# Optimization experiments

Measured on AMD Instinct MI355X. Metric: run time of the kernel, lower is better.

## Reference

```python
import jax, jax.numpy as jnp
import numpy as np

HEADS = 16
HEAD_DIM = 64
EMB = 1024
B, S = 4, 2048
SCALE = 1.0 / 8.0  # fixed constant in the original code
MASK_PENALTY = -50.0  # original adds -50 * upper_triangular, not -inf


def setup_inputs() -> dict:
    key = jax.random.key(0)
    ks = jax.random.split(key, 5)
    x = jax.random.normal(ks[0], (B, S, EMB), dtype=jnp.float32)
    Wq = jax.random.normal(ks[1], (EMB, HEADS * HEAD_DIM), dtype=jnp.float32) * 0.02
    Wk = jax.random.normal(ks[2], (EMB, HEADS * HEAD_DIM), dtype=jnp.float32) * 0.02
    Wv = jax.random.normal(ks[3], (EMB, HEADS * HEAD_DIM), dtype=jnp.float32) * 0.02
    Wr = jax.random.normal(ks[4], (HEADS * HEAD_DIM, EMB), dtype=jnp.float32) * 0.02
    return {"x": x, "Wq": Wq, "Wk": Wk, "Wv": Wv, "Wr": Wr}


def reference(x, Wq, Wk, Wv, Wr):
    b, s, _ = x.shape
    # project and split heads: [b, s, h, d]
    q = (x @ Wq).reshape(b, s, HEADS, HEAD_DIM)
    k = (x @ Wk).reshape(b, s, HEADS, HEAD_DIM)
    v = (x @ Wv).reshape(b, s, HEADS, HEAD_DIM)
    # scores: [b, h, s, s]
    scores = SCALE * jnp.einsum('bqhd,bkhd->bhqk', q, k)
    # causal additive mask: -50 on strictly-upper triangle (faithful to original)
    causal = jnp.triu(jnp.ones((s, s), dtype=x.dtype), k=1)
    scores = scores + MASK_PENALTY * causal
    attn = jax.nn.softmax(scores, axis=-1)
    out = jnp.einsum('bhqk,bkhd->bqhd', attn, v).reshape(b, s, HEADS * HEAD_DIM)
    return out @ Wr
```

## Files before the change

### kernel.cpp

```cpp
#include <hip/hip_runtime.h>

typedef _Float16 f16;
typedef _Float16 f16x8 __attribute__((ext_vector_type(8)));
typedef _Float16 f16x4 __attribute__((ext_vector_type(4)));
typedef float f32x4 __attribute__((ext_vector_type(4)));

#define MFMA16(A, B, C) __builtin_amdgcn_mfma_f32_16x16x32_f16((A), (B), (C), 0, 0, 0)

__device__ __forceinline__ void async16(void* lds, const void* gp) {
    __builtin_amdgcn_global_load_lds(
        (__attribute__((address_space(1))) void*)(gp),
        (__attribute__((address_space(3))) void*)(lds), 16, 0, 0);
}

__global__ __launch_bounds__(256) void k_convert(const float* __restrict__ in,
                                                 f16* __restrict__ out, int n) {
    int i = (blockIdx.x * 256 + threadIdx.x) * 4;
    if (i + 3 < n) {
        float4 v = *(const float4*)(in + i);
        f16x4 o = {(f16)v.x, (f16)v.y, (f16)v.z, (f16)v.w};
        *(f16x4*)(out + i) = o;
    }
}

__global__ __launch_bounds__(256) void k_transpose_w4(const float* __restrict__ Wq,
                                                      const float* __restrict__ Wk,
                                                      const float* __restrict__ Wv,
                                                      const float* __restrict__ Wr,
                                                      f16* __restrict__ Wqkvt,
                                                      f16* __restrict__ Wrt) {
    __shared__ float tile[32][33];
    int z = blockIdx.z;
    const float* W = (z == 0) ? Wq : (z == 1) ? Wk : (z == 2) ? Wv : Wr;
    f16* Wt = (z == 3) ? Wrt : Wqkvt + z * 1048576;
    int c0 = blockIdx.x * 32, r0 = blockIdx.y * 32;
    int tx = threadIdx.x, ty = threadIdx.y;
#pragma unroll
    for (int j = 0; j < 32; j += 8)
        tile[ty + j][tx] = W[(r0 + ty + j) * 1024 + c0 + tx];
    __syncthreads();
#pragma unroll
    for (int j = 0; j < 32; j += 8)
        Wt[(c0 + ty + j) * 1024 + r0 + tx] = (f16)tile[tx][ty + j];
}

__global__ __launch_bounds__(256) void k_transpose_v(const f16* __restrict__ QKV,
                                                     f16* __restrict__ Vt) {
    __shared__ f16 tile[32][33];
    int s0 = blockIdx.x * 32;
    int d0 = blockIdx.y * 32;
    int bh = blockIdx.z;
    int b = bh >> 4, h = bh & 15;
    int tx = threadIdx.x, ty = threadIdx.y;
#pragma unroll
    for (int j = 0; j < 32; j += 8)
        tile[ty + j][tx] = QKV[(b * 2048 + s0 + ty + j) * 3072 + 2048 + h * 64 + d0 + tx];
    __syncthreads();
#pragma unroll
    for (int j = 0; j < 32; j += 8)
        Vt[(bh * 64 + d0 + ty + j) * 2048 + s0 + tx] = tile[tx][ty + j];
}

template <bool OUT_F16>
__global__ __launch_bounds__(256) void k_gemm_bt(const f16* __restrict__ A,
                                                 const f16* __restrict__ Bt,
                                                 void* __restrict__ Cv,
                                                 int M, int N, int K) {
    __shared__ f16 As[128][32];
    __shared__ f16 Bs[128][32];
    int t = threadIdx.x;
    int lane = t & 63, w = t >> 6;
    int wm = (w >> 1) * 64, wn = (w & 1) * 64;
    int m0 = blockIdx.y * 128, n0 = blockIdx.x * 128;
    int ln = lane & 15, g = lane >> 4;

    int lin0 = w * 128 + lane, lin1 = lin0 + 64;
    int r0 = lin0 >> 2, c0 = (lin0 & 3) ^ ((r0 >> 1) & 3);
    int r1 = lin1 >> 2, c1 = (lin1 & 3) ^ ((r1 >> 1) & 3);
    const f16* gA0 = A + (size_t)(m0 + r0) * K + c0 * 8;
    const f16* gA1 = A + (size_t)(m0 + r1) * K + c1 * 8;
    const f16* gB0 = Bt + (size_t)(n0 + r0) * K + c0 * 8;
    const f16* gB1 = Bt + (size_t)(n0 + r1) * K + c1 * 8;
    f16* lA0 = &As[0][0] + w * 1024;
    f16* lB0 = &Bs[0][0] + w * 1024;

    f32x4 acc[4][4] = {};
    int sw = (ln >> 1) & 3;

    for (int k0 = 0; k0 < K; k0 += 32) {
        __syncthreads();
        async16(lA0, gA0 + k0);
        async16(lA0 + 512, gA1 + k0);
        async16(lB0, gB0 + k0);
        async16(lB0 + 512, gB1 + k0);
        __syncthreads();
        f16x8 af[4], bf[4];
#pragma unroll
        for (int i = 0; i < 4; i++) {
            af[i] = *(const f16x8*)&As[wm + i * 16 + ln][(g ^ sw) * 8];
            bf[i] = *(const f16x8*)&Bs[wn + i * 16 + ln][(g ^ sw) * 8];
        }
#pragma unroll
        for (int mt = 0; mt < 4; mt++)
#pragma unroll
            for (int nt = 0; nt < 4; nt++)
                acc[mt][nt] = MFMA16(af[mt], bf[nt], acc[mt][nt]);
    }

    int rg = g * 4;
#pragma unroll
    for (int mt = 0; mt < 4; mt++)
#pragma unroll
        for (int nt = 0; nt < 4; nt++)
#pragma unroll
            for (int r = 0; r < 4; r++) {
                int row = m0 + wm + mt * 16 + rg + r;
                int col = n0 + wn + nt * 16 + ln;
                float v = acc[mt][nt][r];
                if (OUT_F16)
                    ((f16*)Cv)[(size_t)row * N + col] = (f16)v;
                else
                    ((float*)Cv)[(size_t)row * N + col] = v;
            }
}

__global__ __launch_bounds__(256, 2) void k_attn(const f16* __restrict__ QKV,
                                                 const f16* __restrict__ Vt,
                                                 f16* __restrict__ Opart,
                                                 float* __restrict__ Rsum) {
    __shared__ f16 Ks[2][64][64];
    __shared__ f16 Vs[2][64][64];
    int bh = blockIdx.x, pi = blockIdx.y;
    int b = bh >> 4, h = bh & 15;
    int t = threadIdx.x, lane = t & 63, wq = t >> 6;
    int ln = lane & 15, g = lane >> 4, g8 = g * 8, rg = g * 4;
    int sx = ln & 7;

    int r0 = wq * 8 + (lane >> 3);
    int cp = lane & 7;
    int cl = (cp ^ (r0 & 7)) * 8;
    int gk0 = ((r0 & 16) >> 2) | ((r0 & 12) << 1) | (r0 & 3);
    const f16* Kb = QKV + (size_t)b * 2048 * 3072 + 1024 + h * 64;
    const f16* Vb = Vt + (size_t)bh * 64 * 2048;
    const f16* gK0 = Kb + (size_t)gk0 * 3072 + cl;
    const f16* gK1 = Kb + (size_t)(gk0 + 32) * 3072 + cl;
    const f16* gV0 = Vb + (size_t)r0 * 2048 + cl;
    const f16* gV1 = Vb + (size_t)(r0 + 32) * 2048 + cl;

    const float C_SCL = 0.18033688f;
    const float C_MSK = -72.134752f;
    f16x8 ones;
#pragma unroll
    for (int j = 0; j < 8; j++) ones[j] = (f16)1.f;

    int nk0 = 16 - pi;

#define ISSUE(bi, j)                                                      \
    do {                                                                  \
        int jj = (j);                                                     \
        int kt_ = (jj < nk0) ? jj : jj - nk0 + pi + 1;                    \
        size_t kO = (size_t)kt_ * 64;                                     \
        async16(&Ks[bi][wq * 8][0],      gK0 + kO * 3072);                \
        async16(&Ks[bi][32 + wq * 8][0], gK1 + kO * 3072);                \
        async16(&Vs[bi][wq * 8][0],      gV0 + kO);                       \
        async16(&Vs[bi][32 + wq * 8][0], gV1 + kO);                       \
    } while (0)

    ISSUE(0, 0);
    __syncthreads();

    int i = 0;
    for (int phase = 0; phase < 2; phase++) {
        int qt  = phase ? pi : 15 - pi;
        int ktB = phase ? pi + 1 : 0;
        int ktE = phase ? 2 * pi + 2 : 16 - pi;
        int q0 = qt * 128;

        f16x8 bq[2][2];
#pragma unroll
        for (int nt = 0; nt < 2; nt++)
#pragma unroll
            for (int kd = 0; kd < 2; kd++)
                bq[nt][kd] = *(const f16x8*)(QKV +
                    (size_t)(b * 2048 + q0 + wq * 32 + nt * 16 + ln) * 3072 +
                    h * 64 + kd * 32 + g8);

        f32x4 oacc[2][4] = {};
        f32x4 osum[2] = {};

        for (int kt = ktB; kt < ktE; kt++, i++) {
            int cur = i & 1;
            int k0 = kt * 64;
            bool active = (k0 <= q0 + wq * 32 + 31);

            if (i + 1 < 17) ISSUE(cur ^ 1, i + 1);

            if (active) {
                f16x8 ak[2][4];
#pragma unroll
                for (int kd = 0; kd < 2; kd++)
#pragma unroll
                    for (int mt = 0; mt < 4; mt++)
                        ak[kd][mt] = *(const f16x8*)
                            &Ks[cur][mt * 16 + ln][((kd * 4 + g) ^ sx) * 8];
                f32x4 sacc[4][2] = {};
#pragma unroll
                for (int kd = 0; kd < 2; kd++)
#pragma unroll
                    for (int mt = 0; mt < 4; mt++)
#pragma unroll
                        for (int nt = 0; nt < 2; nt++)
                            sacc[mt][nt] = MFMA16(ak[kd][mt], bq[nt][kd], sacc[mt][nt]);

                bool needs_mask = (k0 + 63 > q0 + wq * 32);
                f16x8 ap[2][2];
#pragma unroll
                for (int nt = 0; nt < 2; nt++) {
                    int q = q0 + wq * 32 + nt * 16 + ln;
#pragma unroll
                    for (int mt = 0; mt < 4; mt++) {
                        int kb = mt >> 1, hi4 = (mt & 1) * 4;
#pragma unroll
                        for (int r = 0; r < 4; r++) {
                            float e;
                            if (needs_mask) {
                                int kk = k0 + kb * 32 + hi4 + 8 * g + r;
                                e = __builtin_amdgcn_exp2f(
                                    fmaf(sacc[mt][nt][r], C_SCL, (kk > q) ? C_MSK : 0.f));
                            } else {
                                e = __builtin_amdgcn_exp2f(sacc[mt][nt][r] * C_SCL);
                            }
                            ap[nt][kb][hi4 + r] = (f16)e;
                        }
                    }
                }

#pragma unroll
                for (int kk = 0; kk < 2; kk++) {
                    f16x8 bv[4];
#pragma unroll
                    for (int dt = 0; dt < 4; dt++)
                        bv[dt] = *(const f16x8*)
                            &Vs[cur][dt * 16 + ln][((kk * 4 + g) ^ sx) * 8];
#pragma unroll
                    for (int nt = 0; nt < 2; nt++) {
#pragma unroll
                        for (int dt = 0; dt < 4; dt++)
                            oacc[nt][dt] = MFMA16(ap[nt][kk], bv[dt], oacc[nt][dt]);
                        osum[nt] = MFMA16(ap[nt][kk], ones, osum[nt]);
                    }
                }
            }
            __syncthreads();
        }

        int u = (bh * 16 + qt) * 2 + phase;
#pragma unroll
        for (int nt = 0; nt < 2; nt++)
#pragma unroll
            for (int r = 0; r < 4; r++) {
                float rs = osum[nt][r];
                float inv = __builtin_amdgcn_rcpf(fmaxf(rs, 1e-30f));
                int q = wq * 32 + nt * 16 + rg + r;
                if (ln == 0) Rsum[u * 128 + q] = rs;
#pragma unroll
                for (int dt = 0; dt < 4; dt++)
                    Opart[(size_t)u * 8192 + q * 64 + dt * 16 + ln] =
                        (f16)(oacc[nt][dt][r] * inv);
            }
    }
#undef ISSUE
}

__global__ __launch_bounds__(256) void k_merge(const f16* __restrict__ Op,
                                               const float* __restrict__ Rs,
                                               f16* __restrict__ Ob) {
    int idx = blockIdx.x * 256 + threadIdx.x;
    int d8 = idx & 7;
    int q  = (idx >> 3) & 127;
    int qt = (idx >> 10) & 15;
    int bh = idx >> 14;
    int b = bh >> 4, hd = bh & 15;
    int u0 = (bh * 16 + qt) * 2;
    float rs0 = Rs[u0 * 128 + q], rs1 = Rs[(u0 + 1) * 128 + q];
    float inv = __builtin_amdgcn_rcpf(rs0 + rs1);
    f16x8 o0 = *(const f16x8*)(Op + (size_t)u0 * 8192 + q * 64 + d8 * 8);
    f16x8 o1 = *(const f16x8*)(Op + (size_t)(u0 + 1) * 8192 + q * 64 + d8 * 8);
    f16x8 o;
#pragma unroll
    for (int j = 0; j < 8; j++)
        o[j] = (f16)((rs0 * (float)o0[j] + rs1 * (float)o1[j]) * inv);
    *(f16x8*)(Ob + (size_t)(b * 2048 + qt * 128 + q) * 1024 + hd * 64 + d8 * 8) = o;
}

extern "C" void kernel_launch(void* const* d_in, const int* in_sizes, int n_in,
                              void* d_out, int out_size, void* d_ws, size_t ws_size,
                              hipStream_t stream) {
    const float* x = (const float*)d_in[0];
    const float* Wq = (const float*)d_in[1];
    const float* Wk = (const float*)d_in[2];
    const float* Wv = (const float*)d_in[3];
    const float* Wr = (const float*)d_in[4];
    float* out = (float*)d_out;

    f16* ws = (f16*)d_ws;
    f16* xb    = ws;
    f16* Wqkvt = xb + 8388608;
    f16* Wrt   = Wqkvt + 3145728;
    f16* QKVb  = Wrt + 1048576;
    f16* Vtb   = QKVb + 25165824;
    f16* Obuf  = Vtb + 8388608;
    f16* Opart = Obuf + 8388608;
    float* Rsum = (float*)(Opart + 16777216);

    k_convert<<<8192, 256, 0, stream>>>(x, xb, 8388608);
    dim3 tb(32, 8);
    k_transpose_w4<<<dim3(32, 32, 4), tb, 0, stream>>>(Wq, Wk, Wv, Wr, Wqkvt, Wrt);
    k_gemm_bt<true><<<dim3(24, 64), 256, 0, stream>>>(xb, Wqkvt, QKVb, 8192, 3072, 1024);
    k_transpose_v<<<dim3(64, 2, 64), tb, 0, stream>>>(QKVb, Vtb);
    k_attn<<<dim3(64, 16), 256, 0, stream>>>(QKVb, Vtb, Opart, Rsum);
    k_merge<<<4096, 256, 0, stream>>>(Opart, Rsum, Obuf);
    k_gemm_bt<false><<<dim3(8, 64), 256, 0, stream>>>(Obuf, Wrt, out, 8192, 1024, 1024);
}
```

Before: 285.5 us.

## Double-buffer GEMM LDS tiles and merge input conversion kernels

The GEMM now uses two LDS buffers and issues the asynchronous global-to-LDS loads for the next K slice before running the MFMAs on the current one, with one barrier per iteration instead of two. This is meant to hide global load latency behind compute. Separately, the x conversion and the weight transpose kernels are fused into one launch to remove a kernel launch gap. Double buffering doubles LDS use per block, which may lower occupancy. The next slice's loads may not be guaranteed complete before the barrier without an explicit vmcnt wait.

```diff
diff --git a/kernel.cpp b/kernel.cpp
--- a/kernel.cpp
+++ b/kernel.cpp
@@ -13,35 +13,37 @@
         (__attribute__((address_space(3))) void*)(lds), 16, 0, 0);
 }
 
-__global__ __launch_bounds__(256) void k_convert(const float* __restrict__ in,
-                                                 f16* __restrict__ out, int n) {
-    int i = (blockIdx.x * 256 + threadIdx.x) * 4;
-    if (i + 3 < n) {
-        float4 v = *(const float4*)(in + i);
+__global__ __launch_bounds__(256) void k_prep(const float* __restrict__ x,
+                                              const float* __restrict__ Wq,
+                                              const float* __restrict__ Wk,
+                                              const float* __restrict__ Wv,
+                                              const float* __restrict__ Wr,
+                                              f16* __restrict__ xb,
+                                              f16* __restrict__ Wqkvt,
+                                              f16* __restrict__ Wrt) {
+    __shared__ float tile[32][33];
+    int bid = blockIdx.x;
+    if (bid < 8192) {
+        int i = (bid * 256 + threadIdx.x) * 4;
+        float4 v = *(const float4*)(x + i);
         f16x4 o = {(f16)v.x, (f16)v.y, (f16)v.z, (f16)v.w};
-        *(f16x4*)(out + i) = o;
+        *(f16x4*)(xb + i) = o;
+    } else {
+        int wid = bid - 8192;
+        int z = wid >> 10;
+        int tid = wid & 1023;
+        const float* W = (z == 0) ? Wq : (z == 1) ? Wk : (z == 2) ? Wv : Wr;
+        f16* Wt = (z == 3) ? Wrt : Wqkvt + z * 1048576;
+        int c0 = (tid & 31) * 32, r0 = (tid >> 5) * 32;
+        int tx = threadIdx.x & 31, ty = threadIdx.x >> 5;
+#pragma unroll
+        for (int j = 0; j < 32; j += 8)
+            tile[ty + j][tx] = W[(r0 + ty + j) * 1024 + c0 + tx];
+        __syncthreads();
+#pragma unroll
+        for (int j = 0; j < 32; j += 8)
+            Wt[(c0 + ty + j) * 1024 + r0 + tx] = (f16)tile[tx][ty + j];
     }
-}
-
-__global__ __launch_bounds__(256) void k_transpose_w4(const float* __restrict__ Wq,
-                                                      const float* __restrict__ Wk,
-                                                      const float* __restrict__ Wv,
-                                                      const float* __restrict__ Wr,
-                                                      f16* __restrict__ Wqkvt,
-                                                      f16* __restrict__ Wrt) {
-    __shared__ float tile[32][33];
-    int z = blockIdx.z;
-    const float* W = (z == 0) ? Wq : (z == 1) ? Wk : (z == 2) ? Wv : Wr;
-    f16* Wt = (z == 3) ? Wrt : Wqkvt + z * 1048576;
-    int c0 = blockIdx.x * 32, r0 = blockIdx.y * 32;
-    int tx = threadIdx.x, ty = threadIdx.y;
-#pragma unroll
-    for (int j = 0; j < 32; j += 8)
-        tile[ty + j][tx] = W[(r0 + ty + j) * 1024 + c0 + tx];
-    __syncthreads();
-#pragma unroll
-    for (int j = 0; j < 32; j += 8)
-        Wt[(c0 + ty + j) * 1024 + r0 + tx] = (f16)tile[tx][ty + j];
 }
 
 __global__ __launch_bounds__(256) void k_transpose_v(const f16* __restrict__ QKV,
@@ -66,8 +68,8 @@
                                                  const f16* __restrict__ Bt,
                                                  void* __restrict__ Cv,
                                                  int M, int N, int K) {
-    __shared__ f16 As[128][32];
-    __shared__ f16 Bs[128][32];
+    __shared__ f16 As[2][128][32];
+    __shared__ f16 Bs[2][128][32];
     int t = threadIdx.x;
     int lane = t & 63, w = t >> 6;
     int wm = (w >> 1) * 64, wn = (w & 1) * 64;
@@ -81,31 +83,41 @@
     const f16* gA1 = A + (size_t)(m0 + r1) * K + c1 * 8;
     const f16* gB0 = Bt + (size_t)(n0 + r0) * K + c0 * 8;
     const f16* gB1 = Bt + (size_t)(n0 + r1) * K + c1 * 8;
-    f16* lA0 = &As[0][0] + w * 1024;
-    f16* lB0 = &Bs[0][0] + w * 1024;
 
     f32x4 acc[4][4] = {};
     int sw = (ln >> 1) & 3;
 
+#define GISSUE(bi, kk)                                    \
+    do {                                                  \
+        f16* lA = &As[bi][0][0] + w * 1024;               \
+        f16* lB = &Bs[bi][0][0] + w * 1024;               \
+        async16(lA, gA0 + (kk));                          \
+        async16(lA + 512, gA1 + (kk));                    \
+        async16(lB, gB0 + (kk));                          \
+        async16(lB + 512, gB1 + (kk));                    \
+    } while (0)
+
+    GISSUE(0, 0);
+    __syncthreads();
+
+    int cur = 0;
     for (int k0 = 0; k0 < K; k0 += 32) {
-        __syncthreads();
-        async16(lA0, gA0 + k0);
-        async16(lA0 + 512, gA1 + k0);
-        async16(lB0, gB0 + k0);
-        async16(lB0 + 512, gB1 + k0);
-        __syncthreads();
+        if (k0 + 32 < K) GISSUE(cur ^ 1, k0 + 32);
         f16x8 af[4], bf[4];
 #pragma unroll
         for (int i = 0; i < 4; i++) {
-            af[i] = *(const f16x8*)&As[wm + i * 16 + ln][(g ^ sw) * 8];
-            bf[i] = *(const f16x8*)&Bs[wn + i * 16 + ln][(g ^ sw) * 8];
+            af[i] = *(const f16x8*)&As[cur][wm + i * 16 + ln][(g ^ sw) * 8];
+            bf[i] = *(const f16x8*)&Bs[cur][wn + i * 16 + ln][(g ^ sw) * 8];
         }
 #pragma unroll
         for (int mt = 0; mt < 4; mt++)
 #pragma unroll
             for (int nt = 0; nt < 4; nt++)
                 acc[mt][nt] = MFMA16(af[mt], bf[nt], acc[mt][nt]);
+        __syncthreads();
+        cur ^= 1;
     }
+#undef GISSUE
 
     int rg = g * 4;
 #pragma unroll
@@ -313,10 +325,9 @@
     f16* Opart = Obuf + 8388608;
     float* Rsum = (float*)(Opart + 16777216);
 
-    k_convert<<<8192, 256, 0, stream>>>(x, xb, 8388608);
+    k_prep<<<12288, 256, 0, stream>>>(x, Wq, Wk, Wv, Wr, xb, Wqkvt, Wrt);
+    k_gemm_bt<true><<<dim3(24, 64), 256, 0, stream>>>(xb, Wqkvt, QKVb, 8192, 3072, 1024);
     dim3 tb(32, 8);
-    k_transpose_w4<<<dim3(32, 32, 4), tb, 0, stream>>>(Wq, Wk, Wv, Wr, Wqkvt, Wrt);
-    k_gemm_bt<true><<<dim3(24, 64), 256, 0, stream>>>(xb, Wqkvt, QKVb, 8192, 3072, 1024);
     k_transpose_v<<<dim3(64, 2, 64), tb, 0, stream>>>(QKVb, Vtb);
     k_attn<<<dim3(64, 16), 256, 0, stream>>>(QKVb, Vtb, Opart, Rsum);
     k_merge<<<4096, 256, 0, stream>>>(Opart, Rsum, Obuf);
```

Result: faster. 272.5 us (-4.5%).
